# Performance work log

Hardware: AMD Instinct MI355X
Metric: run time of the kernel (lower is better)

Reference implementation:

```python
import jax, jax.numpy as jnp
import numpy as np

VOCAB = 16000
DIM = 1024
B, T = 4, 2048


def setup_inputs() -> dict:
    key = jax.random.key(0)
    k_ids, k_emb, k_w, k_lw, k_lb = jax.random.split(key, 5)
    input_ids = jax.random.randint(k_ids, (B, T), 0, VOCAB)
    embed = jax.random.normal(k_emb, (VOCAB, DIM), dtype=jnp.float32)
    # w_state = I + 0.05 * (default Linear init ~ U(-1/sqrt(dim), 1/sqrt(dim)))
    bound = 1.0 / np.sqrt(DIM)
    w_state = jnp.eye(DIM, dtype=jnp.float32) + 0.05 * jax.random.uniform(
        k_w, (DIM, DIM), minval=-bound, maxval=bound, dtype=jnp.float32)
    lm_w = jax.random.uniform(k_lw, (VOCAB, DIM), minval=-bound, maxval=bound, dtype=jnp.float32)
    lm_b = jax.random.uniform(k_lb, (VOCAB,), minval=-bound, maxval=bound, dtype=jnp.float32)
    return {"input_ids": input_ids, "embed": embed, "w_state": w_state,
            "lm_w": lm_w, "lm_b": lm_b}


def reference(input_ids, embed, w_state, lm_w, lm_b):
    # h: [B, T, D]
    h = embed[input_ids]
    state0 = jnp.zeros((h.shape[0], h.shape[2]), dtype=h.dtype)

    def step(state, h_t):
        # nn.Linear: state @ W^T ; then add input injection
        new_state = state @ w_state.T + h_t
        return new_state, new_state

    # scan over time: inputs [T, B, D]
    _, outs = jax.lax.scan(step, state0, jnp.swapaxes(h, 0, 1))
    hidden = jnp.swapaxes(outs, 0, 1)  # [B, T, D]
    logits = hidden @ lm_w.T + lm_b    # [B, T, V]
    return logits
```

## Files before the change

### kernel.cpp

```cpp
#include <hip/hip_runtime.h>
#include <hip/hip_bf16.h>
#include <stdint.h>

#define DD 1024
#define BB 4
#define TT 2048
#define VV 16000
#define LCH 4
#define NR 2048
#define PADR 1024
#define NPAD 16128
#define M1C ((size_t)DD * DD)

typedef __bf16 bf16_t;
typedef float f32x4_t __attribute__((ext_vector_type(4)));
typedef bf16_t bf16x8_t __attribute__((ext_vector_type(8)));
typedef bf16_t bf16x4_t __attribute__((ext_vector_type(4)));

#define KIND_SQ 0
#define KIND_ROUND 1
#define KIND_LEVEL 2
#define KIND_CARRY 3

__device__ __forceinline__ void gload16(const void* g, void* l) {
  __builtin_amdgcn_global_load_lds((const __attribute__((address_space(1))) void*)g,
                                   (__attribute__((address_space(3))) void*)l, 16, 0, 0);
}

__global__ __launch_bounds__(256) void k_cvt(const float* __restrict__ src,
                                             bf16_t* __restrict__ dst, int n4) {
  int i = blockIdx.x * blockDim.x + threadIdx.x;
  int stride = gridDim.x * blockDim.x;
  for (; i < n4; i += stride) {
    float4 v = ((const float4*)src)[i];
    union { ushort4 u; bf16_t h[4]; } p;
    p.h[0] = (bf16_t)v.x; p.h[1] = (bf16_t)v.y;
    p.h[2] = (bf16_t)v.z; p.h[3] = (bf16_t)v.w;
    ((ushort4*)dst)[i] = p.u;
  }
}

struct JobF {
  const float* A; const float* B; float* C; const float* Cin;
  int kind; int dlt;
};
struct JobsF { JobF j[8]; };

__global__ __launch_bounds__(256) void k_gatherF(const float* __restrict__ embed,
                                                 const int* __restrict__ ids,
                                                 float* __restrict__ slab0) {
  int r = blockIdx.x;
  int b = r & 3, c = r >> 2;
  int id = ids[b * TT + c * LCH];
  const float4* s = (const float4*)(embed + (size_t)id * DD);
  float4* d = (float4*)(slab0 + (size_t)r * DD);
  for (int i = threadIdx.x; i < DD / 4; i += blockDim.x) d[i] = s[i];
}

template <int NS>
__device__ __forceinline__ void swrite(char* base, int byteoff, float4 v) {
  float r0 = v.x, r1 = v.y, r2 = v.z, r3 = v.w;
#pragma unroll
  for (int p = 0; p < NS; ++p) {
    bf16x4_t h;
    h[0] = (bf16_t)r0; h[1] = (bf16_t)r1; h[2] = (bf16_t)r2; h[3] = (bf16_t)r3;
    *(bf16x4_t*)(base + p * 5120 + byteoff) = h;
    if (p + 1 < NS) {
      r0 -= (float)h[0]; r1 -= (float)h[1]; r2 -= (float)h[2]; r3 -= (float)h[3];
    }
  }
}

template <int NS, bool NN, int MODE>
__device__ __forceinline__ void mbodyF(bf16_t* __restrict__ SBb, const JobF& jb,
                                       const float* __restrict__ embed,
                                       const int* __restrict__ ids,
                                       bf16_t* __restrict__ hidden) {
  const float* A = jb.A;
  const float* Bm = jb.B;
  const int tid = threadIdx.x, lane = tid & 63, wave = tid >> 6;
  const int i0 = blockIdx.y * 64, j0 = blockIdx.x * 64;
  const int wm = (wave >> 1) * 32, wn = (wave & 1) * 32;
  char* Ap = (char*)SBb;
  char* Bp = Ap + NS * 5120;
  const int arow = tid >> 2;
  const int akb = (tid & 3) * 8;
  const int bj = tid & 63, bk4 = (tid >> 6) * 4;
  const int frow = lane & 15, fkb = (lane >> 4) * 16;
  f32x4_t acc[2][2] = {};

  const float* Aptr = A + (size_t)(i0 + arow) * DD + (tid & 3) * 4;
  const float* BptrNT = Bm + (size_t)(j0 + arow) * DD + (tid & 3) * 4;
  const float* BptrNN = Bm + (size_t)bk4 * DD + j0 + bj;

  float4 a0 = *(const float4*)(Aptr);
  float4 a1 = *(const float4*)(Aptr + 16);
  float4 b0, b1;
  float s0[4], s1[4];
  if (!NN) {
    b0 = *(const float4*)(BptrNT);
    b1 = *(const float4*)(BptrNT + 16);
  } else {
#pragma unroll
    for (int s = 0; s < 4; ++s) s0[s] = BptrNN[(size_t)s * DD];
#pragma unroll
    for (int s = 0; s < 4; ++s) s1[s] = BptrNN[(size_t)(16 + s) * DD];
  }

  for (int k0 = 0;;) {
    __syncthreads();
    swrite<NS>(Ap, arow * 80 + akb, a0);
    swrite<NS>(Ap, arow * 80 + akb + 32, a1);
    if (!NN) {
      swrite<NS>(Bp, arow * 80 + akb, b0);
      swrite<NS>(Bp, arow * 80 + akb + 32, b1);
    } else {
      float4 t0; t0.x = s0[0]; t0.y = s0[1]; t0.z = s0[2]; t0.w = s0[3];
      float4 t1; t1.x = s1[0]; t1.y = s1[1]; t1.z = s1[2]; t1.w = s1[3];
      swrite<NS>(Bp, bj * 80 + bk4 * 2, t0);
      swrite<NS>(Bp, bj * 80 + bk4 * 2 + 32, t1);
    }
    __syncthreads();
    int kn = k0 + 32;
    if (kn < DD) {
      a0 = *(const float4*)(Aptr + kn);
      a1 = *(const float4*)(Aptr + kn + 16);
      if (!NN) {
        b0 = *(const float4*)(BptrNT + kn);
        b1 = *(const float4*)(BptrNT + kn + 16);
      } else {
#pragma unroll
        for (int s = 0; s < 4; ++s) s0[s] = BptrNN[(size_t)(kn + s) * DD];
#pragma unroll
        for (int s = 0; s < 4; ++s) s1[s] = BptrNN[(size_t)(kn + 16 + s) * DD];
      }
    }
    bf16x8_t af[NS][2], bfx[NS][2];
#pragma unroll
    for (int p = 0; p < NS; ++p)
#pragma unroll
      for (int mf = 0; mf < 2; ++mf) {
        af[p][mf] = *(const bf16x8_t*)(Ap + p * 5120 + (wm + mf * 16 + frow) * 80 + fkb);
        bfx[p][mf] = *(const bf16x8_t*)(Bp + p * 5120 + (wn + mf * 16 + frow) * 80 + fkb);
      }
#pragma unroll
    for (int pa = 0; pa < NS; ++pa)
#pragma unroll
      for (int pb = 0; pb < NS; ++pb) {
        if (pa + pb < NS) {
#pragma unroll
          for (int mf = 0; mf < 2; ++mf)
#pragma unroll
            for (int nf = 0; nf < 2; ++nf)
              acc[mf][nf] = __builtin_amdgcn_mfma_f32_16x16x32_bf16(
                  af[pa][mf], bfx[pb][nf], acc[mf][nf], 0, 0, 0);
        }
      }
    k0 = kn;
    if (k0 >= DD) break;
  }

  const int ecol = lane & 15, er4 = (lane >> 4) * 4;
#pragma unroll
  for (int mf = 0; mf < 2; ++mf) {
#pragma unroll
    for (int nf = 0; nf < 2; ++nf) {
      const int rb = i0 + wm + mf * 16 + er4;
      const int cj = j0 + wn + nf * 16 + ecol;
#pragma unroll
      for (int rg = 0; rg < 4; ++rg) {
        const int ri = rb + rg;
        float v = acc[mf][nf][rg];
        if (MODE == 0) {
          jb.C[(size_t)ri * DD + cj] = v;
        } else if (MODE == 1) {
          int b = ri & 3, c = ri >> 2, t = c * LCH + jb.dlt;
          v += embed[(size_t)ids[b * TT + t] * DD + cj];
          jb.C[(size_t)ri * DD + cj] = v;
        } else if (MODE == 2) {
          v += jb.Cin[(size_t)ri * DD + cj];
          jb.C[(size_t)ri * DD + cj] = v;
        } else {
          int b = ri & 3, c = ri >> 2, t = c * LCH + jb.dlt;
          hidden[((size_t)b * TT + t) * DD + cj] =
              (bf16_t)(v + jb.Cin[(size_t)ri * DD + cj]);
        }
      }
    }
  }
}

__global__ __launch_bounds__(256, 2) void k_multiF(JobsF jobs,
                                                   const float* __restrict__ embed,
                                                   const int* __restrict__ ids,
                                                   bf16_t* __restrict__ hidden) {
  __shared__ __align__(16) bf16_t SBb[6 * 2560];
  const JobF& jb = jobs.j[blockIdx.z];
  if (jb.kind == KIND_SQ) {
    if (blockIdx.y >= 16) return;
    mbodyF<3, true, 0>(SBb, jb, embed, ids, hidden);
  } else if (jb.kind == KIND_ROUND)
    mbodyF<2, false, 1>(SBb, jb, embed, ids, hidden);
  else if (jb.kind == KIND_LEVEL)
    mbodyF<2, false, 2>(SBb, jb, embed, ids, hidden);
  else
    mbodyF<2, false, 3>(SBb, jb, embed, ids, hidden);
}

#define NTK 32

__global__ __launch_bounds__(512, 2) void k_lmhead2(
    const bf16_t* __restrict__ Ah, const bf16_t* __restrict__ Bw,
    const float* __restrict__ bias, float* __restrict__ Cout) {
  __shared__ __align__(16) char LB[4 * 32768];
  const int tid = threadIdx.x, lane = tid & 63, wave = tid >> 6;
  const int wr = wave >> 2, wc = wave & 3;
  int orig = blockIdx.y * gridDim.x + blockIdx.x;
  int swz = (orig & 7) * 252 + (orig >> 3);
  int by = swz / 63, bx = swz % 63;
  const int m0 = by * 256, n0 = bx * 256;

  const int srow = tid >> 2;
  const int scb = (tid & 3) * 16;

  auto stage = [&](int t) {
    char* buf = LB + (size_t)(t & 3) * 32768;
#pragma unroll
    for (int p = 0; p < 2; ++p) {
      int row = p * 128 + srow;
      int sw = ((row >> 1) & 3) << 4;
      gload16((const char*)Ah + ((size_t)(m0 + row) * DD + t * 32) * 2 + (scb ^ sw),
              buf + p * 8192 + wave * 1024);
      gload16((const char*)Bw + ((size_t)(n0 + row) * DD + t * 32) * 2 + (scb ^ sw),
              buf + 16384 + p * 8192 + wave * 1024);
    }
  };

  const int frow = lane & 15;
  const int c4b = (lane >> 4) * 16;
  f32x4_t acc[8][4] = {};

  stage(0); stage(1); stage(2);
  asm volatile("s_waitcnt vmcnt(8)\ns_barrier" ::: "memory");

  for (int t = 0; t < NTK; ++t) {
    char* Abuf = LB + (size_t)(t & 3) * 32768;
    char* Bbuf = Abuf + 16384;
    if (t + 3 < NTK) stage(t + 3);
    bf16x8_t afr[4], bfr[4];
#pragma unroll
    for (int nf = 0; nf < 4; ++nf) {
      int r = wc * 64 + nf * 16 + frow;
      bfr[nf] = *(const bf16x8_t*)(Bbuf + r * 64 + (c4b ^ (((r >> 1) & 3) << 4)));
    }
#pragma unroll
    for (int mf = 0; mf < 4; ++mf) {
      int r = wr * 128 + mf * 16 + frow;
      afr[mf] = *(const bf16x8_t*)(Abuf + r * 64 + (c4b ^ (((r >> 1) & 3) << 4)));
    }
    __builtin_amdgcn_s_setprio(1);
#pragma unroll
    for (int mf = 0; mf < 4; ++mf)
#pragma unroll
      for (int nf = 0; nf < 4; ++nf)
        acc[mf][nf] = __builtin_amdgcn_mfma_f32_16x16x32_bf16(
            afr[mf], bfr[nf], acc[mf][nf], 0, 0, 0);
    __builtin_amdgcn_s_setprio(0);
#pragma unroll
    for (int mf = 0; mf < 4; ++mf) {
      int r = wr * 128 + 64 + mf * 16 + frow;
      afr[mf] = *(const bf16x8_t*)(Abuf + r * 64 + (c4b ^ (((r >> 1) & 3) << 4)));
    }
    __builtin_amdgcn_s_setprio(1);
#pragma unroll
    for (int mf = 0; mf < 4; ++mf)
#pragma unroll
      for (int nf = 0; nf < 4; ++nf)
        acc[4 + mf][nf] = __builtin_amdgcn_mfma_f32_16x16x32_bf16(
            afr[mf], bfr[nf], acc[4 + mf][nf], 0, 0, 0);
    __builtin_amdgcn_s_setprio(0);
    if (t < NTK - 3) {
      asm volatile("s_waitcnt vmcnt(8)\ns_barrier" ::: "memory");
    } else if (t == NTK - 3) {
      asm volatile("s_waitcnt vmcnt(4)\ns_barrier" ::: "memory");
    } else if (t == NTK - 2) {
      asm volatile("s_waitcnt vmcnt(0)\ns_barrier" ::: "memory");
    }
  }

  const int ecol = lane & 15, er4 = (lane >> 4) * 4;
#pragma unroll
  for (int mf = 0; mf < 8; ++mf) {
#pragma unroll
    for (int nf = 0; nf < 4; ++nf) {
      int gm = m0 + wr * 128 + mf * 16 + er4;
      int gn = n0 + wc * 64 + nf * 16 + ecol;
      if (gn < VV) {
        float bv = bias[gn];
#pragma unroll
        for (int rg = 0; rg < 4; ++rg)
          Cout[(size_t)(gm + rg) * VV + gn] = acc[mf][nf][rg] + bv;
      }
    }
  }
}

extern "C" void kernel_launch(void* const* d_in, const int* in_sizes, int n_in,
                              void* d_out, int out_size, void* d_ws, size_t ws_size,
                              hipStream_t stream) {
  (void)in_sizes; (void)n_in; (void)out_size; (void)ws_size;
  const int* ids = (const int*)d_in[0];
  const float* embed = (const float*)d_in[1];
  const float* w_state = (const float*)d_in[2];
  const float* lm_w = (const float*)d_in[3];
  const float* lm_b = (const float*)d_in[4];
  float* out = (float*)d_out;

  const size_t M1 = M1C;
  float* POW = (float*)d_ws;
  float* LOC = POW + 11 * M1;
  float* E0 = LOC + 8 * M1;
  float* E1 = E0 + 3 * M1;
  bf16_t* HID = (bf16_t*)(E1 + 3 * M1);
  bf16_t* LWB = HID + 8 * M1;
  float* E0d = E0 + (size_t)PADR * DD;
  float* E1d = E1 + (size_t)PADR * DD;

  k_cvt<<<2048, 256, 0, stream>>>(lm_w, LWB, VV * DD / 4);
  hipMemsetAsync(LWB + (size_t)VV * DD, 0,
                 (size_t)(NPAD - VV) * DD * sizeof(bf16_t), stream);
  k_gatherF<<<NR, 256, 0, stream>>>(embed, ids, LOC);
  hipMemsetAsync(E0, 0, (size_t)PADR * DD * sizeof(float), stream);
  hipMemsetAsync(E1, 0, (size_t)PADR * DD * sizeof(float), stream);

  JobsF J{};
  J.j[0] = JobF{w_state, w_state, POW, nullptr, KIND_SQ, 0};
  J.j[1] = JobF{LOC, w_state, LOC + 2 * M1, nullptr, KIND_ROUND, 1};
  k_multiF<<<dim3(16, 32, 2), 256, 0, stream>>>(J, embed, ids, HID);
  J.j[0] = JobF{POW, w_state, POW + M1, nullptr, KIND_SQ, 0};
  J.j[1] = JobF{POW, POW, POW + 2 * M1, nullptr, KIND_SQ, 0};
  J.j[2] = JobF{LOC + 2 * M1, w_state, LOC + 4 * M1, nullptr, KIND_ROUND, 2};
  k_multiF<<<dim3(16, 32, 3), 256, 0, stream>>>(J, embed, ids, HID);
  J.j[0] = JobF{POW + 2 * M1, POW + 2 * M1, POW + 3 * M1, nullptr, KIND_SQ, 0};
  J.j[1] = JobF{LOC + 4 * M1, w_state, LOC + 6 * M1, nullptr, KIND_ROUND, 3};
  k_multiF<<<dim3(16, 32, 2), 256, 0, stream>>>(J, embed, ids, HID);

  hipMemcpyAsync(E0d, LOC + 6 * M1, 2 * M1 * sizeof(float),
                 hipMemcpyDeviceToDevice, stream);

  float* inp = E0d;
  float* outp = E1d;
  for (int k = 0; k < 9; ++k) {
    JobsF J2{};
    int nz = 0;
    J2.j[nz++] = JobF{inp - (size_t)(4 << k) * DD, POW + (size_t)(k + 2) * M1,
                      outp, inp, KIND_LEVEL, 0};
    if (k <= 6)
      J2.j[nz++] = JobF{POW + (size_t)(k + 3) * M1, POW + (size_t)(k + 3) * M1,
                        POW + (size_t)(k + 4) * M1, nullptr, KIND_SQ, 0};
    k_multiF<<<dim3(16, 32, nz), 256, 0, stream>>>(J2, embed, ids, HID);
    float* t = inp; inp = outp; outp = t;
  }

  JobsF Jc{};
  Jc.j[0] = JobF{inp - (size_t)4 * DD, w_state, nullptr, LOC, KIND_CARRY, 0};
  for (int d = 1; d < LCH; ++d)
    Jc.j[d] = JobF{inp - (size_t)4 * DD, POW + (size_t)(d - 1) * M1, nullptr,
                   LOC + (size_t)d * 2 * M1, KIND_CARRY, d};
  k_multiF<<<dim3(16, 32, LCH), 256, 0, stream>>>(Jc, embed, ids, HID);

  dim3 gl(NPAD / 256, (BB * TT) / 256);
  k_lmhead2<<<gl, 512, 0, stream>>>(HID, LWB, lm_b, out);
}
```

Measured before the change: 892.6 us.

## Enlarge split-bf16 GEMM block tile from 64x64 to 128x128

The multi-job split-precision GEMM kernel now computes 128x128 output tiles per block, with each wave owning a 64x64 sub-tile (4x4 MFMA fragments) instead of 32x32. Each staged K-slab of A and B is reused across more MFMAs, cutting shared-memory and global traffic per flop. Grids shrink to 8x16 blocks per job. This lowers parallelism: about 128 blocks per job on a 256-CU part. It also raises register pressure from 16 accumulators plus the bf16 split fragments, which may limit occupancy under the 2-blocks launch bound.

```diff
diff --git a/kernel.cpp b/kernel.cpp
--- a/kernel.cpp
+++ b/kernel.cpp
@@ -57,6 +57,8 @@
   for (int i = threadIdx.x; i < DD / 4; i += blockDim.x) d[i] = s[i];
 }
 
+#define PS128 (128 * 80)
+
 template <int NS>
 __device__ __forceinline__ void swrite(char* base, int byteoff, float4 v) {
   float r0 = v.x, r1 = v.y, r2 = v.z, r3 = v.w;
@@ -64,7 +66,7 @@
   for (int p = 0; p < NS; ++p) {
     bf16x4_t h;
     h[0] = (bf16_t)r0; h[1] = (bf16_t)r1; h[2] = (bf16_t)r2; h[3] = (bf16_t)r3;
-    *(bf16x4_t*)(base + p * 5120 + byteoff) = h;
+    *(bf16x4_t*)(base + p * PS128 + byteoff) = h;
     if (p + 1 < NS) {
       r0 -= (float)h[0]; r1 -= (float)h[1]; r2 -= (float)h[2]; r3 -= (float)h[3];
     }
@@ -79,69 +81,77 @@
   const float* A = jb.A;
   const float* Bm = jb.B;
   const int tid = threadIdx.x, lane = tid & 63, wave = tid >> 6;
-  const int i0 = blockIdx.y * 64, j0 = blockIdx.x * 64;
-  const int wm = (wave >> 1) * 32, wn = (wave & 1) * 32;
+  const int i0 = blockIdx.y * 128, j0 = blockIdx.x * 128;
+  const int wm = (wave >> 1) * 64, wn = (wave & 1) * 64;
   char* Ap = (char*)SBb;
-  char* Bp = Ap + NS * 5120;
+  char* Bp = Ap + NS * PS128;
   const int arow = tid >> 2;
   const int akb = (tid & 3) * 8;
-  const int bj = tid & 63, bk4 = (tid >> 6) * 4;
+  const int bj = tid & 127, bkg = (tid >> 7) * 4;
   const int frow = lane & 15, fkb = (lane >> 4) * 16;
-  f32x4_t acc[2][2] = {};
+  f32x4_t acc[4][4] = {};
 
   const float* Aptr = A + (size_t)(i0 + arow) * DD + (tid & 3) * 4;
+  const float* Aptr1 = Aptr + (size_t)64 * DD;
   const float* BptrNT = Bm + (size_t)(j0 + arow) * DD + (tid & 3) * 4;
-  const float* BptrNN = Bm + (size_t)bk4 * DD + j0 + bj;
-
-  float4 a0 = *(const float4*)(Aptr);
-  float4 a1 = *(const float4*)(Aptr + 16);
-  float4 b0, b1;
-  float s0[4], s1[4];
-  if (!NN) {
-    b0 = *(const float4*)(BptrNT);
-    b1 = *(const float4*)(BptrNT + 16);
-  } else {
-#pragma unroll
-    for (int s = 0; s < 4; ++s) s0[s] = BptrNN[(size_t)s * DD];
-#pragma unroll
-    for (int s = 0; s < 4; ++s) s1[s] = BptrNN[(size_t)(16 + s) * DD];
-  }
-
-  for (int k0 = 0;;) {
-    __syncthreads();
+  const float* BptrNT1 = BptrNT + (size_t)64 * DD;
+  const float* BptrNN = Bm + (size_t)bkg * DD + j0 + bj;
+
+  float4 a0, a1, a2, a3, b0, b1, b2, b3;
+  float s[16];
+
+  auto gld = [&](int k0) {
+    a0 = *(const float4*)(Aptr + k0);
+    a1 = *(const float4*)(Aptr + k0 + 16);
+    a2 = *(const float4*)(Aptr1 + k0);
+    a3 = *(const float4*)(Aptr1 + k0 + 16);
+    if (!NN) {
+      b0 = *(const float4*)(BptrNT + k0);
+      b1 = *(const float4*)(BptrNT + k0 + 16);
+      b2 = *(const float4*)(BptrNT1 + k0);
+      b3 = *(const float4*)(BptrNT1 + k0 + 16);
+    } else {
+#pragma unroll
+      for (int q = 0; q < 4; ++q)
+#pragma unroll
+        for (int e = 0; e < 4; ++e)
+          s[q * 4 + e] = BptrNN[(size_t)(k0 + q * 8 + e) * DD];
+    }
+  };
+  auto stg = [&]() {
     swrite<NS>(Ap, arow * 80 + akb, a0);
     swrite<NS>(Ap, arow * 80 + akb + 32, a1);
+    swrite<NS>(Ap, (64 + arow) * 80 + akb, a2);
+    swrite<NS>(Ap, (64 + arow) * 80 + akb + 32, a3);
     if (!NN) {
       swrite<NS>(Bp, arow * 80 + akb, b0);
       swrite<NS>(Bp, arow * 80 + akb + 32, b1);
+      swrite<NS>(Bp, (64 + arow) * 80 + akb, b2);
+      swrite<NS>(Bp, (64 + arow) * 80 + akb + 32, b3);
     } else {
-      float4 t0; t0.x = s0[0]; t0.y = s0[1]; t0.z = s0[2]; t0.w = s0[3];
-      float4 t1; t1.x = s1[0]; t1.y = s1[1]; t1.z = s1[2]; t1.w = s1[3];
-      swrite<NS>(Bp, bj * 80 + bk4 * 2, t0);
-      swrite<NS>(Bp, bj * 80 + bk4 * 2 + 32, t1);
-    }
+#pragma unroll
+      for (int q = 0; q < 4; ++q) {
+        float4 t;
+        t.x = s[q * 4 + 0]; t.y = s[q * 4 + 1];
+        t.z = s[q * 4 + 2]; t.w = s[q * 4 + 3];
+        swrite<NS>(Bp, bj * 80 + (bkg + q * 8) * 2, t);
+      }
+    }
+  };
+
+  gld(0);
+  for (int kt = 0; kt < 32; ++kt) {
     __syncthreads();
-    int kn = k0 + 32;
-    if (kn < DD) {
-      a0 = *(const float4*)(Aptr + kn);
-      a1 = *(const float4*)(Aptr + kn + 16);
-      if (!NN) {
-        b0 = *(const float4*)(BptrNT + kn);
-        b1 = *(const float4*)(BptrNT + kn + 16);
-      } else {
-#pragma unroll
-        for (int s = 0; s < 4; ++s) s0[s] = BptrNN[(size_t)(kn + s) * DD];
-#pragma unroll
-        for (int s = 0; s < 4; ++s) s1[s] = BptrNN[(size_t)(kn + 16 + s) * DD];
-      }
-    }
-    bf16x8_t af[NS][2], bfx[NS][2];
+    stg();
+    __syncthreads();
+    if (kt + 1 < 32) gld((kt + 1) * 32);
+    bf16x8_t af[NS][4], bfx[NS][4];
 #pragma unroll
     for (int p = 0; p < NS; ++p)
 #pragma unroll
-      for (int mf = 0; mf < 2; ++mf) {
-        af[p][mf] = *(const bf16x8_t*)(Ap + p * 5120 + (wm + mf * 16 + frow) * 80 + fkb);
-        bfx[p][mf] = *(const bf16x8_t*)(Bp + p * 5120 + (wn + mf * 16 + frow) * 80 + fkb);
+      for (int mf = 0; mf < 4; ++mf) {
+        af[p][mf] = *(const bf16x8_t*)(Ap + p * PS128 + (wm + mf * 16 + frow) * 80 + fkb);
+        bfx[p][mf] = *(const bf16x8_t*)(Bp + p * PS128 + (wn + mf * 16 + frow) * 80 + fkb);
       }
 #pragma unroll
     for (int pa = 0; pa < NS; ++pa)
@@ -149,22 +159,20 @@
       for (int pb = 0; pb < NS; ++pb) {
         if (pa + pb < NS) {
 #pragma unroll
-          for (int mf = 0; mf < 2; ++mf)
-#pragma unroll
-            for (int nf = 0; nf < 2; ++nf)
+          for (int mf = 0; mf < 4; ++mf)
+#pragma unroll
+            for (int nf = 0; nf < 4; ++nf)
               acc[mf][nf] = __builtin_amdgcn_mfma_f32_16x16x32_bf16(
                   af[pa][mf], bfx[pb][nf], acc[mf][nf], 0, 0, 0);
         }
       }
-    k0 = kn;
-    if (k0 >= DD) break;
   }
 
   const int ecol = lane & 15, er4 = (lane >> 4) * 4;
 #pragma unroll
-  for (int mf = 0; mf < 2; ++mf) {
-#pragma unroll
-    for (int nf = 0; nf < 2; ++nf) {
+  for (int mf = 0; mf < 4; ++mf) {
+#pragma unroll
+    for (int nf = 0; nf < 4; ++nf) {
       const int rb = i0 + wm + mf * 16 + er4;
       const int cj = j0 + wn + nf * 16 + ecol;
 #pragma unroll
@@ -194,10 +202,10 @@
                                                    const float* __restrict__ embed,
                                                    const int* __restrict__ ids,
                                                    bf16_t* __restrict__ hidden) {
-  __shared__ __align__(16) bf16_t SBb[6 * 2560];
+  __shared__ __align__(16) bf16_t SBb[3 * PS128];
   const JobF& jb = jobs.j[blockIdx.z];
   if (jb.kind == KIND_SQ) {
-    if (blockIdx.y >= 16) return;
+    if (blockIdx.y >= 8) return;
     mbodyF<3, true, 0>(SBb, jb, embed, ids, hidden);
   } else if (jb.kind == KIND_ROUND)
     mbodyF<2, false, 1>(SBb, jb, embed, ids, hidden);
@@ -336,14 +344,14 @@
   JobsF J{};
   J.j[0] = JobF{w_state, w_state, POW, nullptr, KIND_SQ, 0};
   J.j[1] = JobF{LOC, w_state, LOC + 2 * M1, nullptr, KIND_ROUND, 1};
-  k_multiF<<<dim3(16, 32, 2), 256, 0, stream>>>(J, embed, ids, HID);
+  k_multiF<<<dim3(8, 16, 2), 256, 0, stream>>>(J, embed, ids, HID);
   J.j[0] = JobF{POW, w_state, POW + M1, nullptr, KIND_SQ, 0};
   J.j[1] = JobF{POW, POW, POW + 2 * M1, nullptr, KIND_SQ, 0};
   J.j[2] = JobF{LOC + 2 * M1, w_state, LOC + 4 * M1, nullptr, KIND_ROUND, 2};
-  k_multiF<<<dim3(16, 32, 3), 256, 0, stream>>>(J, embed, ids, HID);
+  k_multiF<<<dim3(8, 16, 3), 256, 0, stream>>>(J, embed, ids, HID);
   J.j[0] = JobF{POW + 2 * M1, POW + 2 * M1, POW + 3 * M1, nullptr, KIND_SQ, 0};
   J.j[1] = JobF{LOC + 4 * M1, w_state, LOC + 6 * M1, nullptr, KIND_ROUND, 3};
-  k_multiF<<<dim3(16, 32, 2), 256, 0, stream>>>(J, embed, ids, HID);
+  k_multiF<<<dim3(8, 16, 2), 256, 0, stream>>>(J, embed, ids, HID);
 
   hipMemcpyAsync(E0d, LOC + 6 * M1, 2 * M1 * sizeof(float),
                  hipMemcpyDeviceToDevice, stream);
@@ -358,7 +366,7 @@
     if (k <= 6)
       J2.j[nz++] = JobF{POW + (size_t)(k + 3) * M1, POW + (size_t)(k + 3) * M1,
                         POW + (size_t)(k + 4) * M1, nullptr, KIND_SQ, 0};
-    k_multiF<<<dim3(16, 32, nz), 256, 0, stream>>>(J2, embed, ids, HID);
+    k_multiF<<<dim3(8, 16, nz), 256, 0, stream>>>(J2, embed, ids, HID);
     float* t = inp; inp = outp; outp = t;
   }
 
@@ -367,7 +375,7 @@
   for (int d = 1; d < LCH; ++d)
     Jc.j[d] = JobF{inp - (size_t)4 * DD, POW + (size_t)(d - 1) * M1, nullptr,
                    LOC + (size_t)d * 2 * M1, KIND_CARRY, d};
-  k_multiF<<<dim3(16, 32, LCH), 256, 0, stream>>>(Jc, embed, ids, HID);
+  k_multiF<<<dim3(8, 16, LCH), 256, 0, stream>>>(Jc, embed, ids, HID);
 
   dim3 gl(NPAD / 256, (BB * TT) / 256);
   k_lmhead2<<<gl, 512, 0, stream>>>(HID, LWB, lm_b, out);
```

Measured after the change: 1.120 ms. 1.25x slower.
